# Kernel tuning notes

Hardware: AMD Instinct MI355X
Metric: run time of the kernel (lower is better)

Reference implementation:

```python
import jax, jax.numpy as jnp
import numpy as np

B, T, F, U = 64, 512, 1024, 256


def setup_inputs() -> dict:
    key = jax.random.key(0)
    ks = jax.random.split(key, 9)
    x = jax.random.normal(ks[0], (B, T, F), dtype=jnp.float32)
    # variable-length sequences, zero-padded tail (Masking layer semantics)
    lengths = jax.random.randint(ks[1], (B,), T // 2, T + 1)
    valid = (jnp.arange(T)[None, :] < lengths[:, None]).astype(jnp.float32)
    x = x * valid[:, :, None]
    s_fc = 1.0 / np.sqrt(F)
    s_u = 1.0 / np.sqrt(U)
    W_fc = jax.random.uniform(ks[2], (F, U), jnp.float32, -s_fc, s_fc)
    b_fc = jnp.zeros((U,), jnp.float32)
    W_x = jax.random.uniform(ks[3], (U, 4 * U), jnp.float32, -s_u, s_u)
    W_h = jax.random.uniform(ks[4], (U, 4 * U), jnp.float32, -s_u, s_u)
    # Keras unit_forget_bias: ones for forget-gate slice, zeros elsewhere
    b_lstm = jnp.concatenate([jnp.zeros((U,)), jnp.ones((U,)), jnp.zeros((2 * U,))]).astype(jnp.float32)
    W_p = jax.random.uniform(ks[5], (U, 1), jnp.float32, -s_u, s_u)
    b_p = jnp.zeros((1,), jnp.float32)
    return {"inputs": x, "W_fc": W_fc, "b_fc": b_fc, "W_x": W_x,
            "W_h": W_h, "b_lstm": b_lstm, "W_p": W_p, "b_p": b_p}


def _forward(inputs, W_fc, b_fc, W_x, W_h, b_lstm, W_p, b_p):
    # Masking layer: timestep masked iff ALL features == 0.0
    mask = jnp.any(inputs != 0.0, axis=-1)              # [B, T] bool
    x = inputs * mask[:, :, None].astype(inputs.dtype)  # Masking zeroes masked steps
    # Dense(units, relu) applied per timestep
    z = jax.nn.relu(jnp.einsum('btf,fu->btu', x, W_fc) + b_fc)  # [B, T, U]

    units = W_h.shape[0]
    h0 = jnp.zeros((x.shape[0], units), x.dtype)
    c0 = jnp.zeros((x.shape[0], units), x.dtype)

    def step(carry, xt_mt):
        h, c = carry
        xt, mt = xt_mt                                   # [B, U], [B]
        gates = xt @ W_x + h @ W_h + b_lstm              # [B, 4U]
        i, f, g, o = jnp.split(gates, 4, axis=-1)
        i = jax.nn.sigmoid(i)
        f = jax.nn.sigmoid(f)
        g = jnp.tanh(g)
        o = jax.nn.sigmoid(o)
        c_new = f * c + i * g
        h_new = o * jnp.tanh(c_new)
        m = mt[:, None]
        # Keras masked-RNN semantics: skip step, carry previous h/c and output
        h2 = jnp.where(m, h_new, h)
        c2 = jnp.where(m, c_new, c)
        return (h2, c2), h2

    z_t = jnp.swapaxes(z, 0, 1)        # [T, B, U]
    m_t = jnp.swapaxes(mask, 0, 1)     # [T, B]
    _, hs = jax.lax.scan(step, (h0, c0), (z_t, m_t))
    hs = jnp.swapaxes(hs, 0, 1)        # [B, T, U]
    # Dense(1, sigmoid) prediction head
    return jax.nn.sigmoid(jnp.einsum('btu,uo->bto', hs, W_p) + b_p)  # [B, T, 1]


def reference(inputs, W_fc, b_fc, W_x, W_h, b_lstm, W_p, b_p):
    return _forward(inputs, W_fc, b_fc, W_x, W_h, b_lstm, W_p, b_p)
```

## Files before the change

### kernel.cpp

```cpp
#include <hip/hip_runtime.h>
#include <hip/hip_fp16.h>
#include <hip/hip_fp8.h>
#include <cstdint>

#define BB 64
#define TT 512
#define FF 1024
#define UU 256
#define GG 1024

typedef _Float16 f16x8 __attribute__((ext_vector_type(8)));
typedef float f32x4 __attribute__((ext_vector_type(4)));
typedef int i32x8 __attribute__((ext_vector_type(8)));

typedef union { uint4 u4[2]; i32x8 v; } pk32;

__device__ __forceinline__ float sigmf_(float x) { return 1.f / (1.f + __expf(-x)); }
__device__ __forceinline__ float tanhf_(float x) { return 1.f - 2.f / (1.f + __expf(2.f * x)); }

__global__ __launch_bounds__(256) void mask_kernel(const float* __restrict__ x,
                                                   float* __restrict__ maskF) {
  int row = blockIdx.x;
  int tid = threadIdx.x;
  const float4* xr = (const float4*)(x + (size_t)row * FF);
  float4 v = xr[tid];
  bool nz = (v.x != 0.f) || (v.y != 0.f) || (v.z != 0.f) || (v.w != 0.f);
  __shared__ int flag;
  if (tid == 0) flag = 0;
  __syncthreads();
  if (__any(nz)) {
    if ((tid & 63) == 0) atomicOr(&flag, 1);
  }
  __syncthreads();
  if (tid == 0) maskF[row] = flag ? 1.f : 0.f;
}

__global__ __launch_bounds__(256) void pack_whP(const float* __restrict__ Wh,
                                                uint8_t* __restrict__ whP) {
  int col = blockIdx.x;
  int k = threadIdx.x;
  __hip_fp8_e4m3 f(Wh[(size_t)k * GG + col] * 16.f);
  whP[col * 256 + k] = (uint8_t)f.__x;
}

template <typename TA, bool RELU, bool PERM>
__global__ __launch_bounds__(256) void gemm16(const TA* __restrict__ A,
                                              const float* __restrict__ Bm,
                                              const float* __restrict__ bias,
                                              __half* __restrict__ C,
                                              int M, int N, int K) {
  __shared__ _Float16 As[128][40];
  __shared__ _Float16 Bs[64][40];
  int tid = threadIdx.x;
  int lane = tid & 63, w = tid >> 6;
  int wm = w & 1, wn = w >> 1;
  int m0 = blockIdx.x * 128, n0 = blockIdx.y * 64;
  int fr = lane & 15, ks = lane >> 4;

  f32x4 acc[4][2];
#pragma unroll
  for (int i = 0; i < 4; ++i)
#pragma unroll
    for (int j = 0; j < 2; ++j) acc[i][j] = (f32x4){0.f, 0.f, 0.f, 0.f};

  for (int k0 = 0; k0 < K; k0 += 32) {
    {
      int r = tid >> 3, kq = (tid & 7) * 4;
#pragma unroll
      for (int i = 0; i < 4; ++i) {
        int row = r + 32 * i;
        const TA* src = A + (size_t)(m0 + row) * K + k0 + kq;
        if constexpr (sizeof(TA) == 4) {
          float4 v = *reinterpret_cast<const float4*>(src);
          union { uint2 u; _Float16 h[4]; } pk;
          pk.h[0] = (_Float16)v.x; pk.h[1] = (_Float16)v.y;
          pk.h[2] = (_Float16)v.z; pk.h[3] = (_Float16)v.w;
          *reinterpret_cast<uint2*>(&As[row][kq]) = pk.u;
        } else {
          uint2 v = *reinterpret_cast<const uint2*>(src);
          *reinterpret_cast<uint2*>(&As[row][kq]) = v;
        }
      }
      int nn = tid & 63, kb = tid >> 6;
#pragma unroll
      for (int i = 0; i < 8; ++i) {
        int kk = kb + 4 * i;
        Bs[nn][kk] = (_Float16)Bm[(size_t)(k0 + kk) * N + n0 + nn];
      }
    }
    __syncthreads();
    f16x8 af[4], bf[2];
#pragma unroll
    for (int fm = 0; fm < 4; ++fm)
      af[fm] = *reinterpret_cast<const f16x8*>(&As[wm * 64 + fm * 16 + fr][ks * 8]);
#pragma unroll
    for (int fn = 0; fn < 2; ++fn)
      bf[fn] = *reinterpret_cast<const f16x8*>(&Bs[wn * 32 + fn * 16 + fr][ks * 8]);
#pragma unroll
    for (int fm = 0; fm < 4; ++fm)
#pragma unroll
      for (int fn = 0; fn < 2; ++fn)
        acc[fm][fn] = __builtin_amdgcn_mfma_f32_16x16x32_f16(af[fm], bf[fn], acc[fm][fn], 0, 0, 0);
    __syncthreads();
  }
#pragma unroll
  for (int fm = 0; fm < 4; ++fm)
#pragma unroll
    for (int fn = 0; fn < 2; ++fn) {
      int mg0 = m0 + wm * 64 + fm * 16 + ks * 4;
      int ng = n0 + wn * 32 + fn * 16 + fr;
      float bv = bias[ng];
      int ngs = PERM ? ((ng & 255) * 4 + (ng >> 8)) : ng;
#pragma unroll
      for (int r = 0; r < 4; ++r) {
        float v = acc[fm][fn][r] + bv;
        if constexpr (RELU) v = fmaxf(v, 0.f);
        C[(size_t)(mg0 + r) * N + ngs] = __float2half(v);
      }
    }
}

__attribute__((amdgpu_waves_per_eu(4, 4)))
__global__ void __launch_bounds__(1024, 1)
lstm_rec(const uint8_t* __restrict__ whP,
         const __half* __restrict__ zxi,
         const float* __restrict__ maskF,
         const float* __restrict__ Wp,
         __half* __restrict__ ppG)
{
  __shared__ __align__(16) uint8_t hpk[2][256];
  __shared__ float mlds[TT];

  const int b = blockIdx.x;
  const int t = threadIdx.x;
  const int lane = t & 63, w = t >> 6;
  const int fr = lane & 15, q = lane >> 4;
  const int SC1 = 0x7F7F7F7F;

  const uint4* whP4 = (const uint4*)whP;

  pk32 bfr[2][4];
#pragma unroll
  for (int kt = 0; kt < 2; ++kt)
#pragma unroll
    for (int ct = 0; ct < 4; ++ct) {
      int col = ct * 256 + w * 16 + fr;
      bfr[kt][ct].u4[0] = whP4[col * 16 + kt * 8 + q * 2];
      bfr[kt][ct].u4[1] = whP4[col * 16 + kt * 8 + q * 2 + 1];
    }
#pragma unroll
  for (int kt = 0; kt < 2; ++kt)
#pragma unroll
    for (int ct = 0; ct < 4; ++ct) {
      asm volatile("" : "+v"(bfr[kt][ct].u4[0].x), "+v"(bfr[kt][ct].u4[0].y),
                        "+v"(bfr[kt][ct].u4[0].z), "+v"(bfr[kt][ct].u4[0].w));
      asm volatile("" : "+v"(bfr[kt][ct].u4[1].x), "+v"(bfr[kt][ct].u4[1].y),
                        "+v"(bfr[kt][ct].u4[1].z), "+v"(bfr[kt][ct].u4[1].w));
    }

  if (t < 64) ((uint32_t*)hpk[0])[t] = 0u;
  if (t < TT) mlds[t] = maskF[b * TT + t];
  float c_state = 0.f, h_state = 0.f;
  float wpv = Wp[w * 16 + fr];
  __syncthreads();

  const uint2* zp = (const uint2*)(zxi + (size_t)b * TT * GG);
  __half* ppp = ppG + (size_t)b * TT * UU;
  const int u = w * 16 + fr;

  uint2 zx_c = zp[u];
  __half pp_prev = __float2half(0.f);

  int p = 0;
  for (int step = 0; step < TT; ++step) {
    if (step > 0 && q == 0) ppp[(size_t)(step - 1) * UU + u] = pp_prev;

    const uint2* zq = zp + ((step + 1 < TT) ? 256 : 0);
    uint2 zx_n = zq[u];
    float mval = mlds[step];

    const uint4* hp4 = (const uint4*)hpk[p];
    f32x4 d0 = {0.f, 0.f, 0.f, 0.f}, d1 = d0, d2 = d0, d3 = d0;
#pragma unroll
    for (int kt = 0; kt < 2; ++kt) {
      pk32 a;
      a.u4[0] = hp4[kt * 8 + q * 2];
      a.u4[1] = hp4[kt * 8 + q * 2 + 1];
      d0 = __builtin_amdgcn_mfma_scale_f32_16x16x128_f8f6f4(
          a.v, bfr[kt][0].v, d0, 0, 0, 0, SC1, 0, SC1);
      d1 = __builtin_amdgcn_mfma_scale_f32_16x16x128_f8f6f4(
          a.v, bfr[kt][1].v, d1, 0, 0, 0, SC1, 0, SC1);
      d2 = __builtin_amdgcn_mfma_scale_f32_16x16x128_f8f6f4(
          a.v, bfr[kt][2].v, d2, 0, 0, 0, SC1, 0, SC1);
      d3 = __builtin_amdgcn_mfma_scale_f32_16x16x128_f8f6f4(
          a.v, bfr[kt][3].v, d3, 0, 0, 0, SC1, 0, SC1);
    }

    {
      union { uint2 u2; __half2 h2[2]; } zz;
      zz.u2 = zx_c;
      float2 zif = __half22float2(zz.h2[0]);
      float2 zgo = __half22float2(zz.h2[1]);
      float gi = fmaf(d0[0], 0.0625f, zif.x);
      float gf = fmaf(d1[0], 0.0625f, zif.y);
      float gg = fmaf(d2[0], 0.0625f, zgo.x);
      float go = fmaf(d3[0], 0.0625f, zgo.y);
      float ig = sigmf_(gi);
      float fg = sigmf_(gf);
      float g_ = tanhf_(gg);
      float og = sigmf_(go);
      float cn = fg * c_state + ig * g_;
      float hn = og * tanhf_(cn);
      bool on = (mval > 0.5f);
      c_state = on ? cn : c_state;
      h_state = on ? hn : h_state;
      __hip_fp8_e4m3 f8(h_state);
      if (q == 0) hpk[p ^ 1][u] = (uint8_t)f8.__x;
      pp_prev = __float2half(h_state * wpv);
    }
    asm volatile("s_waitcnt lgkmcnt(0)" ::: "memory");
    __builtin_amdgcn_s_barrier();
    asm volatile("" ::: "memory");
    p ^= 1;
    zp += 256;
    zx_c = zx_n;
  }
  if (q == 0) ppp[(size_t)(TT - 1) * UU + u] = pp_prev;
}

__global__ __launch_bounds__(256) void proj_kernel(const __half* __restrict__ ppG,
                                                   const float* __restrict__ bp,
                                                   float* __restrict__ out) {
  int row = blockIdx.x * 4 + (threadIdx.x >> 6);
  int lane = threadIdx.x & 63;
  const ushort4* pr = (const ushort4*)(ppG + (size_t)row * UU);
  ushort4 v = pr[lane];
  __half2 a = *reinterpret_cast<__half2*>(&v.x);
  __half2 c = *reinterpret_cast<__half2*>(&v.z);
  float2 af = __half22float2(a), cf = __half22float2(c);
  float s = af.x + af.y + cf.x + cf.y;
#pragma unroll
  for (int off = 32; off > 0; off >>= 1) s += __shfl_down(s, off);
  if (lane == 0) out[row] = 1.f / (1.f + __expf(-(s + bp[0])));
}

extern "C" void kernel_launch(void* const* d_in, const int* in_sizes, int n_in,
                              void* d_out, int out_size, void* d_ws, size_t ws_size,
                              hipStream_t stream) {
  const float* x = (const float*)d_in[0];
  const float* Wfc = (const float*)d_in[1];
  const float* bfc = (const float*)d_in[2];
  const float* Wx = (const float*)d_in[3];
  const float* Wh = (const float*)d_in[4];
  const float* blstm = (const float*)d_in[5];
  const float* Wp = (const float*)d_in[6];
  const float* bp = (const float*)d_in[7];
  float* out = (float*)d_out;

  char* ws = (char*)d_ws;
  float* maskF = (float*)(ws);
  __half* zh = (__half*)(ws + 131072);
  __half* zxi = (__half*)(ws + 131072 + 16777216);
  uint8_t* whP = (uint8_t*)(ws + 131072 + 16777216 + 67108864);
  __half* ppG = zh;

  mask_kernel<<<BB * TT, 256, 0, stream>>>(x, maskF);
  pack_whP<<<GG, 256, 0, stream>>>(Wh, whP);
  gemm16<float, true, false><<<dim3((BB * TT) / 128, UU / 64), 256, 0, stream>>>(
      x, Wfc, bfc, zh, BB * TT, UU, FF);
  gemm16<__half, false, true><<<dim3((BB * TT) / 128, GG / 64), 256, 0, stream>>>(
      zh, Wx, blstm, zxi, BB * TT, GG, UU);
  lstm_rec<<<BB, 1024, 0, stream>>>(whP, zxi, maskF, Wp, ppG);
  proj_kernel<<<(BB * TT) / 4, 256, 0, stream>>>(ppG, bp, out);
}
```

Baseline: 773.7 us.

## Halve LSTM recurrence block to 8 waves, each computing 32 hidden units

```diff
diff --git a/kernel.cpp b/kernel.cpp
--- a/kernel.cpp
+++ b/kernel.cpp
@@ -120,8 +120,8 @@
     }
 }
 
-__attribute__((amdgpu_waves_per_eu(4, 4)))
-__global__ void __launch_bounds__(1024, 1)
+__attribute__((amdgpu_waves_per_eu(2, 2)))
+__global__ void __launch_bounds__(512, 1)
 lstm_rec(const uint8_t* __restrict__ whP,
          const __half* __restrict__ zxi,
          const float* __restrict__ maskF,
@@ -135,76 +135,78 @@
   const int t = threadIdx.x;
   const int lane = t & 63, w = t >> 6;
   const int fr = lane & 15, q = lane >> 4;
+  const int jj = q & 1;
   const int SC1 = 0x7F7F7F7F;
 
   const uint4* whP4 = (const uint4*)whP;
 
-  pk32 bfr[2][4];
+  pk32 bfr[2][8];
 #pragma unroll
   for (int kt = 0; kt < 2; ++kt)
 #pragma unroll
-    for (int ct = 0; ct < 4; ++ct) {
-      int col = ct * 256 + w * 16 + fr;
-      bfr[kt][ct].u4[0] = whP4[col * 16 + kt * 8 + q * 2];
-      bfr[kt][ct].u4[1] = whP4[col * 16 + kt * 8 + q * 2 + 1];
-    }
+    for (int g = 0; g < 4; ++g)
+#pragma unroll
+      for (int j = 0; j < 2; ++j) {
+        int col = g * 256 + w * 32 + j * 16 + fr;
+        bfr[kt][g * 2 + j].u4[0] = whP4[col * 16 + kt * 8 + q * 2];
+        bfr[kt][g * 2 + j].u4[1] = whP4[col * 16 + kt * 8 + q * 2 + 1];
+      }
 #pragma unroll
   for (int kt = 0; kt < 2; ++kt)
 #pragma unroll
-    for (int ct = 0; ct < 4; ++ct) {
-      asm volatile("" : "+v"(bfr[kt][ct].u4[0].x), "+v"(bfr[kt][ct].u4[0].y),
-                        "+v"(bfr[kt][ct].u4[0].z), "+v"(bfr[kt][ct].u4[0].w));
-      asm volatile("" : "+v"(bfr[kt][ct].u4[1].x), "+v"(bfr[kt][ct].u4[1].y),
-                        "+v"(bfr[kt][ct].u4[1].z), "+v"(bfr[kt][ct].u4[1].w));
+    for (int T = 0; T < 8; ++T) {
+      asm volatile("" : "+v"(bfr[kt][T].u4[0].x), "+v"(bfr[kt][T].u4[0].y),
+                        "+v"(bfr[kt][T].u4[0].z), "+v"(bfr[kt][T].u4[0].w));
+      asm volatile("" : "+v"(bfr[kt][T].u4[1].x), "+v"(bfr[kt][T].u4[1].y),
+                        "+v"(bfr[kt][T].u4[1].z), "+v"(bfr[kt][T].u4[1].w));
     }
 
   if (t < 64) ((uint32_t*)hpk[0])[t] = 0u;
-  if (t < TT) mlds[t] = maskF[b * TT + t];
+  mlds[t] = maskF[b * TT + t];
   float c_state = 0.f, h_state = 0.f;
-  float wpv = Wp[w * 16 + fr];
+  const int ue = w * 32 + jj * 16 + fr;
+  float wpv = Wp[ue];
   __syncthreads();
 
   const uint2* zp = (const uint2*)(zxi + (size_t)b * TT * GG);
   __half* ppp = ppG + (size_t)b * TT * UU;
-  const int u = w * 16 + fr;
-
-  uint2 zx_c = zp[u];
+
+  uint2 zx_c = zp[ue];
   __half pp_prev = __float2half(0.f);
 
   int p = 0;
   for (int step = 0; step < TT; ++step) {
-    if (step > 0 && q == 0) ppp[(size_t)(step - 1) * UU + u] = pp_prev;
+    if (step > 0 && lane < 32) ppp[(size_t)(step - 1) * UU + w * 32 + lane] = pp_prev;
 
     const uint2* zq = zp + ((step + 1 < TT) ? 256 : 0);
-    uint2 zx_n = zq[u];
+    uint2 zx_n = zq[ue];
     float mval = mlds[step];
 
     const uint4* hp4 = (const uint4*)hpk[p];
-    f32x4 d0 = {0.f, 0.f, 0.f, 0.f}, d1 = d0, d2 = d0, d3 = d0;
-#pragma unroll
-    for (int kt = 0; kt < 2; ++kt) {
-      pk32 a;
-      a.u4[0] = hp4[kt * 8 + q * 2];
-      a.u4[1] = hp4[kt * 8 + q * 2 + 1];
-      d0 = __builtin_amdgcn_mfma_scale_f32_16x16x128_f8f6f4(
-          a.v, bfr[kt][0].v, d0, 0, 0, 0, SC1, 0, SC1);
-      d1 = __builtin_amdgcn_mfma_scale_f32_16x16x128_f8f6f4(
-          a.v, bfr[kt][1].v, d1, 0, 0, 0, SC1, 0, SC1);
-      d2 = __builtin_amdgcn_mfma_scale_f32_16x16x128_f8f6f4(
-          a.v, bfr[kt][2].v, d2, 0, 0, 0, SC1, 0, SC1);
-      d3 = __builtin_amdgcn_mfma_scale_f32_16x16x128_f8f6f4(
-          a.v, bfr[kt][3].v, d3, 0, 0, 0, SC1, 0, SC1);
-    }
+    pk32 a0, a1;
+    a0.u4[0] = hp4[q * 2];     a0.u4[1] = hp4[q * 2 + 1];
+    a1.u4[0] = hp4[8 + q * 2]; a1.u4[1] = hp4[8 + q * 2 + 1];
+    f32x4 d[8];
+#pragma unroll
+    for (int T = 0; T < 8; ++T) {
+      f32x4 z = {0.f, 0.f, 0.f, 0.f};
+      z = __builtin_amdgcn_mfma_scale_f32_16x16x128_f8f6f4(
+          a0.v, bfr[0][T].v, z, 0, 0, 0, SC1, 0, SC1);
+      d[T] = __builtin_amdgcn_mfma_scale_f32_16x16x128_f8f6f4(
+          a1.v, bfr[1][T].v, z, 0, 0, 0, SC1, 0, SC1);
+    }
+    float s0 = d[0][0], s1 = d[1][0], s2 = d[2][0], s3 = d[3][0];
+    float s4 = d[4][0], s5 = d[5][0], s6 = d[6][0], s7 = d[7][0];
 
     {
       union { uint2 u2; __half2 h2[2]; } zz;
       zz.u2 = zx_c;
       float2 zif = __half22float2(zz.h2[0]);
       float2 zgo = __half22float2(zz.h2[1]);
-      float gi = fmaf(d0[0], 0.0625f, zif.x);
-      float gf = fmaf(d1[0], 0.0625f, zif.y);
-      float gg = fmaf(d2[0], 0.0625f, zgo.x);
-      float go = fmaf(d3[0], 0.0625f, zgo.y);
+      float gi = fmaf(jj ? s1 : s0, 0.0625f, zif.x);
+      float gf = fmaf(jj ? s3 : s2, 0.0625f, zif.y);
+      float gg = fmaf(jj ? s5 : s4, 0.0625f, zgo.x);
+      float go = fmaf(jj ? s7 : s6, 0.0625f, zgo.y);
       float ig = sigmf_(gi);
       float fg = sigmf_(gf);
       float g_ = tanhf_(gg);
@@ -215,7 +217,7 @@
       c_state = on ? cn : c_state;
       h_state = on ? hn : h_state;
       __hip_fp8_e4m3 f8(h_state);
-      if (q == 0) hpk[p ^ 1][u] = (uint8_t)f8.__x;
+      if (lane < 32) hpk[p ^ 1][w * 32 + lane] = (uint8_t)f8.__x;
       pp_prev = __float2half(h_state * wpv);
     }
     asm volatile("s_waitcnt lgkmcnt(0)" ::: "memory");
@@ -225,7 +227,7 @@
     zp += 256;
     zx_c = zx_n;
   }
-  if (q == 0) ppp[(size_t)(TT - 1) * UU + u] = pp_prev;
+  if (lane < 32) ppp[(size_t)(TT - 1) * UU + w * 32 + lane] = pp_prev;
 }
 
 __global__ __launch_bounds__(256) void proj_kernel(const __half* __restrict__ ppG,
@@ -270,6 +272,6 @@
       x, Wfc, bfc, zh, BB * TT, UU, FF);
   gemm16<__half, false, true><<<dim3((BB * TT) / 128, GG / 64), 256, 0, stream>>>(
       zh, Wx, blstm, zxi, BB * TT, GG, UU);
-  lstm_rec<<<BB, 1024, 0, stream>>>(whP, zxi, maskF, Wp, ppG);
+  lstm_rec<<<BB, 512, 0, stream>>>(whP, zxi, maskF, Wp, ppG);
   proj_kernel<<<(BB * TT) / 4, 256, 0, stream>>>(ppG, bp, out);
 }
```

After: 666.8 us. 13.8% less time.
